# Kernel tuning notes

Measured on AMD Instinct MI355X. Metric: run time of the kernel, lower is better.

## Reference

```python
import jax, jax.numpy as jnp
import numpy as np

L, H, A, I, V, B, T = 6, 1024, 1024, 4096, 50277, 4, 2048
EPS = 1e-5
NEG = -1e38  # numerically equivalent to -inf init for the WKV exponent


def setup_inputs() -> dict:
    key = jax.random.key(0)
    ks = iter(jax.random.split(key, 32))
    def nrm(shape, s):
        return jax.random.normal(next(ks), shape, jnp.float32) * s
    def uni(shape):
        return jax.random.uniform(next(ks), shape, jnp.float32)
    inp = {
        'input_ids': jax.random.randint(next(ks), (B, T), 0, V),
        'embed': nrm((V, H), 0.02),
        'pre_ln_w': jnp.ones((H,), jnp.float32), 'pre_ln_b': jnp.zeros((H,), jnp.float32),
        'post_ln_w': jnp.ones((H,), jnp.float32), 'post_ln_b': jnp.zeros((H,), jnp.float32),
        'ln1_w': jnp.ones((L, H), jnp.float32), 'ln1_b': jnp.zeros((L, H), jnp.float32),
        'ln2_w': jnp.ones((L, H), jnp.float32), 'ln2_b': jnp.zeros((L, H), jnp.float32),
        'att_mix_k': uni((L, 1, 1, H)), 'att_mix_v': uni((L, 1, 1, H)), 'att_mix_r': uni((L, 1, 1, H)),
        'att_wk': nrm((L, A, H), H ** -0.5), 'att_wv': nrm((L, A, H), H ** -0.5),
        'att_wr': nrm((L, A, H), H ** -0.5), 'att_wo': nrm((L, H, A), A ** -0.5),
        'time_decay': nrm((L, A), 0.5), 'time_first': nrm((L, A), 0.5),
        'ffn_mix_k': uni((L, 1, 1, H)), 'ffn_mix_r': uni((L, 1, 1, H)),
        'ffn_wk': nrm((L, I, H), H ** -0.5), 'ffn_wr': nrm((L, H, H), H ** -0.5),
        'ffn_wv': nrm((L, H, I), I ** -0.5),
    }
    return inp


def layer_norm(x, w, b):
    mu = jnp.mean(x, axis=-1, keepdims=True)
    var = jnp.var(x, axis=-1, keepdims=True)
    return (x - mu) * jax.lax.rsqrt(var + EPS) * w + b


def time_shift(x):  # previous token, zero at t=0
    return jnp.pad(x, ((0, 0), (1, 0), (0, 0)))[:, :-1]


def wkv_scan(u, w, k, v):
    """RWKV WKV recurrence with max-exponent stabilization.
    u,w: [A]; k,v: [B,T,A] -> [B,T,A]."""
    def step(carry, kv):
        a, b, p = carry           # [B,A] each
        kt, vt = kv               # [B,A]
        q = jnp.maximum(p, u + kt)
        wt = jnp.exp(u + kt - q)
        sc = jnp.exp(p - q)
        out = (a * sc + wt * vt) / (b * sc + wt)
        q2 = jnp.maximum(p + w, kt)
        s1 = jnp.exp(p + w - q2)
        s2 = jnp.exp(kt - q2)
        return (s1 * a + s2 * vt, s1 * b + s2, q2), out
    bsz = k.shape[0]
    init = (jnp.zeros((bsz, A), k.dtype), jnp.zeros((bsz, A), k.dtype),
            jnp.full((bsz, A), NEG, k.dtype))
    _, out = jax.lax.scan(step, init, (k.transpose(1, 0, 2), v.transpose(1, 0, 2)))
    return out.transpose(1, 0, 2)


def reference(input_ids, embed, pre_ln_w, pre_ln_b, post_ln_w, post_ln_b,
              ln1_w, ln1_b, ln2_w, ln2_b,
              att_mix_k, att_mix_v, att_mix_r, att_wk, att_wv, att_wr, att_wo,
              time_decay, time_first, ffn_mix_k, ffn_mix_r, ffn_wk, ffn_wr, ffn_wv):
    h = layer_norm(embed[input_ids], pre_ln_w, pre_ln_b)
    for i in range(L):
        # --- attention (time mixing) ---
        x = layer_norm(h, ln1_w[i], ln1_b[i])
        prev = time_shift(x)
        k = (att_mix_k[i] * x + (1 - att_mix_k[i]) * prev) @ att_wk[i].T
        v = (att_mix_v[i] * x + (1 - att_mix_v[i]) * prev) @ att_wv[i].T
        r = jax.nn.sigmoid((att_mix_r[i] * x + (1 - att_mix_r[i]) * prev) @ att_wr[i].T)
        y = wkv_scan(time_first[i], -jnp.exp(time_decay[i]), k, v)
        h = h + (r * y) @ att_wo[i].T
        # --- feed forward (channel mixing) ---
        x = layer_norm(h, ln2_w[i], ln2_b[i])
        prev = time_shift(x)
        kk = jnp.square(jax.nn.relu((ffn_mix_k[i] * x + (1 - ffn_mix_k[i]) * prev) @ ffn_wk[i].T))
        rr = jax.nn.sigmoid((ffn_mix_r[i] * x + (1 - ffn_mix_r[i]) * prev) @ ffn_wr[i].T)
        h = h + rr * (kk @ ffn_wv[i].T)
    return layer_norm(h, post_ln_w, post_ln_b)
```

## Files before the change

### kernel.cpp

```cpp
#include <hip/hip_runtime.h>
#include <stdint.h>


#define LNUM 6
#define HD   1024
#define AD   1024
#define TT   2048
#define NTOK 8192
#define EPSF 1e-5f
#define NEGF (-1e38f)

#define WKV_C  32
#define WKV_NC 64
#define NCH    4096

typedef __attribute__((ext_vector_type(8))) short bf16x8;
typedef __attribute__((ext_vector_type(4))) float f32x4;

__device__ __forceinline__ unsigned short f2bf(float f) {
  union { float f; uint32_t u; } c; c.f = f;
  uint32_t r = c.u + 0x7fffu + ((c.u >> 16) & 1u);
  return (unsigned short)(r >> 16);
}

__device__ __forceinline__ void gld_lds16(const void* g, const void* l) {
  __builtin_amdgcn_global_load_lds(
      (const __attribute__((address_space(1))) void*)(uintptr_t)g,
      (__attribute__((address_space(3))) void*)(uint32_t)(uintptr_t)l,
      16, 0, 0);
}

enum { EP_NONE = 0, EP_SIG = 1, EP_RELUSQ = 2, EP_ADD = 3, EP_MULADD = 4, EP_KVR = 5 };

template <int EPI>
__global__ __launch_bounds__(256) void gemm_nt(
    const unsigned short* __restrict__ Aact,
    const unsigned short* __restrict__ Bw,
    float* __restrict__ Co,
    unsigned short* __restrict__ Cb,
    const float* __restrict__ aux,
    int K, int M)
{
  __shared__ unsigned short sA[4][128 * 32];
  __shared__ unsigned short sB[4][128 * 32];
  const int tid  = threadIdx.x;
  const int lane = tid & 63;
  const int wave = tid >> 6;
  const int quad = lane >> 4;
  const int r16  = lane & 15;
  const int wm = wave >> 1, wn = wave & 1;
  const int m0 = blockIdx.x * 128;
  const int n0 = blockIdx.y * 128;

  if constexpr (EPI == EP_KVR) {
    const int z = blockIdx.z;
    Aact += (size_t)z * 8388608;
    Bw   += (size_t)z * 1048576;
    Co   += (size_t)z * 8388608;
  }

  f32x4 acc[4][4];
#pragma unroll
  for (int i = 0; i < 4; ++i)
#pragma unroll
    for (int j = 0; j < 4; ++j) acc[i][j] = (f32x4){0.f, 0.f, 0.f, 0.f};

  const int wbase = wave * 64;
  const int nk = K >> 5;

  const int row0 = tid >> 2,         kc0 = tid & 3;
  const int row1 = 64 + row0,        kc1 = kc0;
  const int sw0 = (row0 >> 1) & 3;
  const int kg0 = kc0 ^ sw0;
  const int kg1 = kc1 ^ sw0;

  auto STAGE = [&](int buf, int kt) {
    const int k0 = kt << 5;
    gld_lds16(Aact + (size_t)(m0 + row0) * K + k0 + kg0 * 8,
              (const char*)sA[buf] + wbase * 16);
    gld_lds16(Bw   + (size_t)(n0 + row0) * K + k0 + kg0 * 8,
              (const char*)sB[buf] + wbase * 16);
    gld_lds16(Aact + (size_t)(m0 + row1) * K + k0 + kg1 * 8,
              (const char*)sA[buf] + (256 + wbase) * 16);
    gld_lds16(Bw   + (size_t)(n0 + row1) * K + k0 + kg1 * 8,
              (const char*)sB[buf] + (256 + wbase) * 16);
  };

  STAGE(0, 0);
  if (nk > 1) STAGE(1, 1);

  const int swr = (r16 >> 1) & 3;
  const int qsw = (quad ^ swr) * 8;

  for (int kt = 0; kt < nk; ++kt) {
    if (kt + 2 < nk) {
      STAGE((kt + 2) & 3, kt + 2);
      asm volatile("s_waitcnt vmcnt(8)" ::: "memory");
    } else if (kt + 1 < nk) {
      asm volatile("s_waitcnt vmcnt(4)" ::: "memory");
    } else {
      asm volatile("s_waitcnt vmcnt(0)" ::: "memory");
    }
    __builtin_amdgcn_s_barrier();
    asm volatile("" ::: "memory");

    const unsigned short* a_s = sA[kt & 3];
    const unsigned short* b_s = sB[kt & 3];
    bf16x8 af[4], bfr[4];
#pragma unroll
    for (int i = 0; i < 4; ++i) {
      af[i]  = *(const bf16x8*)(a_s + (wm * 64 + i * 16 + r16) * 32 + qsw);
      bfr[i] = *(const bf16x8*)(b_s + (wn * 64 + i * 16 + r16) * 32 + qsw);
    }
#pragma unroll
    for (int i = 0; i < 4; ++i)
#pragma unroll
      for (int j = 0; j < 4; ++j)
        acc[i][j] = __builtin_amdgcn_mfma_f32_16x16x32_bf16(af[i], bfr[j], acc[i][j], 0, 0, 0);
  }

#pragma unroll
  for (int i = 0; i < 4; ++i) {
    const int ar = m0 + wm * 64 + i * 16 + quad * 4;
#pragma unroll
    for (int j = 0; j < 4; ++j) {
      const int cc = n0 + wn * 64 + j * 16 + r16;
#pragma unroll
      for (int r = 0; r < 4; ++r) {
        const size_t idx = (size_t)(ar + r) * M + cc;
        const float v = acc[i][j][r];
        if constexpr (EPI == EP_NONE)   Co[idx] = v;
        if constexpr (EPI == EP_SIG)    Co[idx] = 1.f / (1.f + __expf(-v));
        if constexpr (EPI == EP_RELUSQ) { const float t = fmaxf(v, 0.f); Cb[idx] = f2bf(t * t); }
        if constexpr (EPI == EP_ADD)    Co[idx] += v;
        if constexpr (EPI == EP_MULADD) Co[idx] += aux[idx] * v;
        if constexpr (EPI == EP_KVR) {
          Co[idx] = (blockIdx.z == 2) ? (1.f / (1.f + __expf(-v))) : v;
        }
      }
    }
  }
}

__global__ __launch_bounds__(256) void ln_kernel(
    const float* __restrict__ in, const int* __restrict__ ids,
    const float* __restrict__ emb,
    const float* __restrict__ gw, const float* __restrict__ gb,
    float* __restrict__ out)
{
  const int n = blockIdx.x, tid = threadIdx.x;
  const float* src = ids ? (emb + (size_t)ids[n] * HD) : (in + (size_t)n * HD);
  const float4 v = ((const float4*)src)[tid];
  float s  = v.x + v.y + v.z + v.w;
  float s2 = v.x * v.x + v.y * v.y + v.z * v.z + v.w * v.w;
#pragma unroll
  for (int off = 32; off > 0; off >>= 1) {
    s  += __shfl_down(s, off);
    s2 += __shfl_down(s2, off);
  }
  __shared__ float red[8];
  const int wv = tid >> 6, ln = tid & 63;
  if (ln == 0) { red[wv] = s; red[4 + wv] = s2; }
  __syncthreads();
  if (tid == 0) {
    const float S  = red[0] + red[1] + red[2] + red[3];
    const float S2 = red[4] + red[5] + red[6] + red[7];
    const float mu = S * (1.f / HD);
    const float var = S2 * (1.f / HD) - mu * mu;
    red[0] = mu; red[1] = rsqrtf(var + EPSF);
  }
  __syncthreads();
  const float mu = red[0], rs = red[1];
  const float4 w4 = ((const float4*)gw)[tid];
  const float4 b4 = ((const float4*)gb)[tid];
  float4 o;
  o.x = (v.x - mu) * rs * w4.x + b4.x;
  o.y = (v.y - mu) * rs * w4.y + b4.y;
  o.z = (v.z - mu) * rs * w4.z + b4.z;
  o.w = (v.w - mu) * rs * w4.w + b4.w;
  ((float4*)(out + (size_t)n * HD))[tid] = o;
}

__global__ __launch_bounds__(256) void lnmix_kernel(
    const float* __restrict__ h,
    const float* __restrict__ gw, const float* __restrict__ gb,
    const float* __restrict__ m0p, const float* __restrict__ m1p, const float* __restrict__ m2p,
    ushort4* __restrict__ o0, ushort4* __restrict__ o1, ushort4* __restrict__ o2)
{
  const int n = blockIdx.x, tid = threadIdx.x;
  const int t = n & (TT - 1);
  const float4 vc = ((const float4*)(h + (size_t)n * HD))[tid];
  float4 vp = make_float4(0.f, 0.f, 0.f, 0.f);
  if (t != 0) vp = ((const float4*)(h + (size_t)(n - 1) * HD))[tid];

  float sc  = vc.x + vc.y + vc.z + vc.w;
  float sc2 = vc.x * vc.x + vc.y * vc.y + vc.z * vc.z + vc.w * vc.w;
  float sp  = vp.x + vp.y + vp.z + vp.w;
  float sp2 = vp.x * vp.x + vp.y * vp.y + vp.z * vp.z + vp.w * vp.w;
#pragma unroll
  for (int off = 32; off > 0; off >>= 1) {
    sc  += __shfl_down(sc, off);
    sc2 += __shfl_down(sc2, off);
    sp  += __shfl_down(sp, off);
    sp2 += __shfl_down(sp2, off);
  }
  __shared__ float red[16];
  const int wv = tid >> 6, ln = tid & 63;
  if (ln == 0) { red[wv] = sc; red[4 + wv] = sc2; red[8 + wv] = sp; red[12 + wv] = sp2; }
  __syncthreads();
  if (tid == 0) {
    float S  = red[0] + red[1] + red[2] + red[3];
    float S2 = red[4] + red[5] + red[6] + red[7];
    float mu = S * (1.f / HD);
    float var = S2 * (1.f / HD) - mu * mu;
    red[0] = mu; red[1] = rsqrtf(var + EPSF);
    S  = red[8] + red[9] + red[10] + red[11];
    S2 = red[12] + red[13] + red[14] + red[15];
    mu = S * (1.f / HD);
    var = S2 * (1.f / HD) - mu * mu;
    red[2] = mu; red[3] = rsqrtf(var + EPSF);
  }
  __syncthreads();
  const float muc = red[0], rsc = red[1];
  const float mup = red[2], rsp = red[3];
  const float4 w4 = ((const float4*)gw)[tid];
  const float4 b4 = ((const float4*)gb)[tid];
  float4 xc, xp;
  xc.x = (vc.x - muc) * rsc * w4.x + b4.x;
  xc.y = (vc.y - muc) * rsc * w4.y + b4.y;
  xc.z = (vc.z - muc) * rsc * w4.z + b4.z;
  xc.w = (vc.w - muc) * rsc * w4.w + b4.w;
  if (t != 0) {
    xp.x = (vp.x - mup) * rsp * w4.x + b4.x;
    xp.y = (vp.y - mup) * rsp * w4.y + b4.y;
    xp.z = (vp.z - mup) * rsp * w4.z + b4.z;
    xp.w = (vp.w - mup) * rsp * w4.w + b4.w;
  } else {
    xp = make_float4(0.f, 0.f, 0.f, 0.f);
  }

  const size_t o = (size_t)n * 256 + tid;
  float4 m = ((const float4*)m0p)[tid];
  ushort4 r;
  r.x = f2bf(m.x * xc.x + (1.f - m.x) * xp.x);
  r.y = f2bf(m.y * xc.y + (1.f - m.y) * xp.y);
  r.z = f2bf(m.z * xc.z + (1.f - m.z) * xp.z);
  r.w = f2bf(m.w * xc.w + (1.f - m.w) * xp.w);
  o0[o] = r;
  m = ((const float4*)m1p)[tid];
  r.x = f2bf(m.x * xc.x + (1.f - m.x) * xp.x);
  r.y = f2bf(m.y * xc.y + (1.f - m.y) * xp.y);
  r.z = f2bf(m.z * xc.z + (1.f - m.z) * xp.z);
  r.w = f2bf(m.w * xc.w + (1.f - m.w) * xp.w);
  o1[o] = r;
  if (o2) {
    m = ((const float4*)m2p)[tid];
    r.x = f2bf(m.x * xc.x + (1.f - m.x) * xp.x);
    r.y = f2bf(m.y * xc.y + (1.f - m.y) * xp.y);
    r.z = f2bf(m.z * xc.z + (1.f - m.z) * xp.z);
    r.w = f2bf(m.w * xc.w + (1.f - m.w) * xp.w);
    o2[o] = r;
  }
}

__global__ __launch_bounds__(256) void wkv_p1(
    const float* __restrict__ kx, const float* __restrict__ vx,
    const float* __restrict__ tdecay,
    float* __restrict__ la, float* __restrict__ lb, float* __restrict__ lp)
{
  const int c = blockIdx.x * 256 + threadIdx.x;
  const int a = c & (AD - 1);
  const int b = c >> 10;
  const int j = blockIdx.y;
  const float w = -__expf(tdecay[a]);
  const size_t base = ((size_t)b * TT + (size_t)j * WKV_C) * AD + a;
  float A = 0.f, Bb = 0.f, p = NEGF;
#pragma unroll 4
  for (int t = 0; t < WKV_C; ++t) {
    const float kt = kx[base + (size_t)t * AD];
    const float vt = vx[base + (size_t)t * AD];
    const float pn = fmaxf(p + w, kt);
    const float s1 = __expf(p + w - pn);
    const float s2 = __expf(kt - pn);
    A = s1 * A + s2 * vt;
    Bb = s1 * Bb + s2;
    p = pn;
  }
  const int o = j * NCH + c;
  la[o] = A; lb[o] = Bb; lp[o] = p;
}

__global__ __launch_bounds__(256) void wkv_p2(
    const float* __restrict__ la, const float* __restrict__ lb,
    const float* __restrict__ lp, const float* __restrict__ tdecay,
    float* __restrict__ sa, float* __restrict__ sb, float* __restrict__ sp)
{
  const int c = blockIdx.x * 256 + threadIdx.x;
  const int a = c & (AD - 1);
  const float wC = -__expf(tdecay[a]) * (float)WKV_C;
  float A = 0.f, Bb = 0.f, p = NEGF;
  for (int j = 0; j < WKV_NC; ++j) {
    const int o = j * NCH + c;
    sa[o] = A; sb[o] = Bb; sp[o] = p;
    const float A2 = la[o], B2 = lb[o], p2 = lp[o];
    const float pn = fmaxf(p + wC, p2);
    const float e1 = __expf(p + wC - pn);
    const float e2 = __expf(p2 - pn);
    A = e1 * A + e2 * A2;
    Bb = e1 * Bb + e2 * B2;
    p = pn;
  }
}

__global__ __launch_bounds__(256) void wkv_p3(
    const float* __restrict__ kx, const float* __restrict__ vx,
    const float* __restrict__ rx,
    const float* __restrict__ tfirst, const float* __restrict__ tdecay,
    const float* __restrict__ sa, const float* __restrict__ sb,
    const float* __restrict__ sp,
    unsigned short* __restrict__ ry)
{
  const int c = blockIdx.x * 256 + threadIdx.x;
  const int a = c & (AD - 1);
  const int b = c >> 10;
  const int j = blockIdx.y;
  const float u = tfirst[a];
  const float w = -__expf(tdecay[a]);
  const size_t base = ((size_t)b * TT + (size_t)j * WKV_C) * AD + a;
  const int o = j * NCH + c;
  float A = sa[o], Bb = sb[o], p = sp[o];
#pragma unroll 2
  for (int t = 0; t < WKV_C; ++t) {
    const size_t off = base + (size_t)t * AD;
    const float kt = kx[off], vt = vx[off];
    const float q  = fmaxf(p, u + kt);
    const float wt = __expf(u + kt - q);
    const float sc = __expf(p - q);
    const float y  = (A * sc + wt * vt) / (Bb * sc + wt);
    ry[off] = f2bf(y * rx[off]);
    const float pn = fmaxf(p + w, kt);
    const float s1 = __expf(p + w - pn);
    const float s2 = __expf(kt - pn);
    A = s1 * A + s2 * vt;
    Bb = s1 * Bb + s2;
    p = pn;
  }
}

__global__ __launch_bounds__(256) void f2b7_kernel(
    const float* __restrict__ s0, const float* __restrict__ s1,
    const float* __restrict__ s2, const float* __restrict__ s3,
    const float* __restrict__ s4, const float* __restrict__ s5,
    const float* __restrict__ s6, ushort4* __restrict__ wb4)
{
  const size_t i = (size_t)blockIdx.x * 256 + threadIdx.x;
  const float* s; size_t rel;
  if      (i <  262144) { s = s0; rel = i; }
  else if (i <  524288) { s = s1; rel = i -  262144; }
  else if (i <  786432) { s = s2; rel = i -  524288; }
  else if (i < 1048576) { s = s3; rel = i -  786432; }
  else if (i < 2097152) { s = s4; rel = i - 1048576; }
  else if (i < 2359296) { s = s5; rel = i - 2097152; }
  else                  { s = s6; rel = i - 2359296; }
  const float4 v = ((const float4*)s)[rel];
  ushort4 r;
  r.x = f2bf(v.x); r.y = f2bf(v.y); r.z = f2bf(v.z); r.w = f2bf(v.w);
  wb4[i] = r;
}

extern "C" void kernel_launch(void* const* d_in, const int* in_sizes, int n_in,
                              void* d_out, int out_size, void* d_ws, size_t ws_size,
                              hipStream_t stream)
{
  (void)in_sizes; (void)n_in; (void)out_size; (void)ws_size;
  const int*   ids   = (const int*)d_in[0];
  const float* emb   = (const float*)d_in[1];
  const float* prew  = (const float*)d_in[2];
  const float* preb  = (const float*)d_in[3];
  const float* postw = (const float*)d_in[4];
  const float* postb = (const float*)d_in[5];
  const float* ln1w  = (const float*)d_in[6];
  const float* ln1b  = (const float*)d_in[7];
  const float* ln2w  = (const float*)d_in[8];
  const float* ln2b  = (const float*)d_in[9];
  const float* amk   = (const float*)d_in[10];
  const float* amv   = (const float*)d_in[11];
  const float* amr   = (const float*)d_in[12];
  const float* awk   = (const float*)d_in[13];
  const float* awv   = (const float*)d_in[14];
  const float* awr   = (const float*)d_in[15];
  const float* awo   = (const float*)d_in[16];
  const float* td    = (const float*)d_in[17];
  const float* tf    = (const float*)d_in[18];
  const float* fmk   = (const float*)d_in[19];
  const float* fmr   = (const float*)d_in[20];
  const float* fwk   = (const float*)d_in[21];
  const float* fwr   = (const float*)d_in[22];
  const float* fwv   = (const float*)d_in[23];

  char* ws = (char*)d_ws;
  float* h  = (float*)(ws + 0);
  float* x  = (float*)(ws + 33554432);
  float* kb = (float*)(ws + 67108864);
  float* vb = (float*)(ws + 100663296);
  float* rb = (float*)(ws + 134217728);
  unsigned short* ab = (unsigned short*)(ws + 167772160);
  unsigned short* wb = (unsigned short*)(ws + 234881024);

  unsigned short* xk = ab;
  unsigned short* xv = ab + 8388608;
  unsigned short* xr = ab + 16777216;
  unsigned short* ry = ab + 25165824;

  float* wla = x;
  float* wlb = x + WKV_NC * NCH;
  float* wlp = x + 2 * WKV_NC * NCH;
  float* wsa = x + 3 * WKV_NC * NCH;
  float* wsb = x + 4 * WKV_NC * NCH;
  float* wsp = x + 5 * WKV_NC * NCH;

  const dim3 blk(256);
  const dim3 g1(NTOK / 128, 1024 / 128);
  const dim3 g2(NTOK / 128, 4096 / 128);
  const dim3 gkvr(NTOK / 128, 1024 / 128, 3);
  const dim3 gw(NCH / 256, WKV_NC);

  ln_kernel<<<NTOK, blk, 0, stream>>>(nullptr, ids, emb, prew, preb, h);

  for (int i = 0; i < LNUM; ++i) {
    f2b7_kernel<<<13312, blk, 0, stream>>>(
        awk + (size_t)i * 1048576, awv + (size_t)i * 1048576,
        awr + (size_t)i * 1048576, awo + (size_t)i * 1048576,
        fwk + (size_t)i * 4194304, fwr + (size_t)i * 1048576,
        fwv + (size_t)i * 4194304, (ushort4*)wb);

    lnmix_kernel<<<NTOK, blk, 0, stream>>>(h, ln1w + i * HD, ln1b + i * HD,
                                           amk + i * HD, amv + i * HD, amr + i * HD,
                                           (ushort4*)xk, (ushort4*)xv, (ushort4*)xr);
    gemm_nt<EP_KVR><<<gkvr, blk, 0, stream>>>(xk, wb, kb, nullptr, nullptr, 1024, 1024);
    wkv_p1<<<gw, blk, 0, stream>>>(kb, vb, td + i * AD, wla, wlb, wlp);
    wkv_p2<<<NCH / 256, blk, 0, stream>>>(wla, wlb, wlp, td + i * AD, wsa, wsb, wsp);
    wkv_p3<<<gw, blk, 0, stream>>>(kb, vb, rb, tf + i * AD, td + i * AD, wsa, wsb, wsp, ry);
    gemm_nt<EP_ADD ><<<g1, blk, 0, stream>>>(ry, wb + 3145728, h, nullptr, nullptr, 1024, 1024);

    lnmix_kernel<<<NTOK, blk, 0, stream>>>(h, ln2w + i * HD, ln2b + i * HD,
                                           fmk + i * HD, fmr + i * HD, nullptr,
                                           (ushort4*)kb, (ushort4*)vb, nullptr);
    gemm_nt<EP_RELUSQ><<<g2, blk, 0, stream>>>((unsigned short*)kb, wb + 4194304, nullptr, ab, nullptr, 1024, 4096);
    gemm_nt<EP_SIG   ><<<g1, blk, 0, stream>>>((unsigned short*)vb, wb + 8388608, rb, nullptr, nullptr, 1024, 1024);
    gemm_nt<EP_MULADD><<<g1, blk, 0, stream>>>(ab, wb + 9437184, h, nullptr, rb, 4096, 1024);
  }

  ln_kernel<<<NTOK, blk, 0, stream>>>(h, nullptr, nullptr, postw, postb, (float*)d_out);
}
```

Baseline: 2.750 ms.

## Use 512-thread GEMM blocks and merge FFN key and receptance GEMMs

The GEMM kernel moves from 256 to 512 threads per 128x128 tile, so each wave computes a 64x32 sub-tile and each thread issues one staging load per operand per k-step, with the vmcnt waits adjusted to match. The aim is more waves per tile to hide latency and fewer accumulator registers per thread. Separately, the FFN relu-squared key GEMM and the sigmoid receptance GEMM are merged into a single launch, with blockIdx.y selecting the operand offsets and epilogue, which saves a launch and lets both fill the device together. The cost is lower MFMA-per-LDS-read reuse per wave and a branchy epilogue.

```diff
diff --git a/kernel.cpp b/kernel.cpp
--- a/kernel.cpp
+++ b/kernel.cpp
@@ -30,10 +30,11 @@
       16, 0, 0);
 }
 
-enum { EP_NONE = 0, EP_SIG = 1, EP_RELUSQ = 2, EP_ADD = 3, EP_MULADD = 4, EP_KVR = 5 };
+enum { EP_NONE = 0, EP_SIG = 1, EP_RELUSQ = 2, EP_ADD = 3, EP_MULADD = 4,
+       EP_KVR = 5, EP_FKR = 6 };
 
 template <int EPI>
-__global__ __launch_bounds__(256) void gemm_nt(
+__global__ __launch_bounds__(512, 4) void gemm_nt(
     const unsigned short* __restrict__ Aact,
     const unsigned short* __restrict__ Bw,
     float* __restrict__ Co,
@@ -48,56 +49,60 @@
   const int wave = tid >> 6;
   const int quad = lane >> 4;
   const int r16  = lane & 15;
-  const int wm = wave >> 1, wn = wave & 1;
+  const int wm = wave >> 2, wn = wave & 3;
   const int m0 = blockIdx.x * 128;
-  const int n0 = blockIdx.y * 128;
-
+  int n0 = blockIdx.y * 128;
+
+  bool sig = false;
   if constexpr (EPI == EP_KVR) {
     const int z = blockIdx.z;
     Aact += (size_t)z * 8388608;
     Bw   += (size_t)z * 1048576;
     Co   += (size_t)z * 8388608;
   }
-
-  f32x4 acc[4][4];
+  if constexpr (EPI == EP_FKR) {
+    if (blockIdx.y >= 32) {
+      sig = true;
+      Aact += 16777216;
+      Bw   += 4194304;
+      n0   = (blockIdx.y - 32) * 128;
+      M    = 1024;
+    } else {
+      M = 4096;
+    }
+  }
+
+  f32x4 acc[4][2];
 #pragma unroll
   for (int i = 0; i < 4; ++i)
 #pragma unroll
-    for (int j = 0; j < 4; ++j) acc[i][j] = (f32x4){0.f, 0.f, 0.f, 0.f};
-
-  const int wbase = wave * 64;
+    for (int j = 0; j < 2; ++j) acc[i][j] = (f32x4){0.f, 0.f, 0.f, 0.f};
+
   const int nk = K >> 5;
 
-  const int row0 = tid >> 2,         kc0 = tid & 3;
-  const int row1 = 64 + row0,        kc1 = kc0;
-  const int sw0 = (row0 >> 1) & 3;
-  const int kg0 = kc0 ^ sw0;
-  const int kg1 = kc1 ^ sw0;
+  const int row0 = tid >> 2, kc0 = tid & 3;
+  const int kg0  = kc0 ^ ((row0 >> 1) & 3);
+  const int wbase = wave * 64 * 16;
 
   auto STAGE = [&](int buf, int kt) {
     const int k0 = kt << 5;
     gld_lds16(Aact + (size_t)(m0 + row0) * K + k0 + kg0 * 8,
-              (const char*)sA[buf] + wbase * 16);
+              (const char*)sA[buf] + wbase);
     gld_lds16(Bw   + (size_t)(n0 + row0) * K + k0 + kg0 * 8,
-              (const char*)sB[buf] + wbase * 16);
-    gld_lds16(Aact + (size_t)(m0 + row1) * K + k0 + kg1 * 8,
-              (const char*)sA[buf] + (256 + wbase) * 16);
-    gld_lds16(Bw   + (size_t)(n0 + row1) * K + k0 + kg1 * 8,
-              (const char*)sB[buf] + (256 + wbase) * 16);
+              (const char*)sB[buf] + wbase);
   };
 
   STAGE(0, 0);
   if (nk > 1) STAGE(1, 1);
 
-  const int swr = (r16 >> 1) & 3;
-  const int qsw = (quad ^ swr) * 8;
+  const int qsw = (quad ^ ((r16 >> 1) & 3)) * 8;
 
   for (int kt = 0; kt < nk; ++kt) {
     if (kt + 2 < nk) {
       STAGE((kt + 2) & 3, kt + 2);
-      asm volatile("s_waitcnt vmcnt(8)" ::: "memory");
+      asm volatile("s_waitcnt vmcnt(4)" ::: "memory");
     } else if (kt + 1 < nk) {
-      asm volatile("s_waitcnt vmcnt(4)" ::: "memory");
+      asm volatile("s_waitcnt vmcnt(2)" ::: "memory");
     } else {
       asm volatile("s_waitcnt vmcnt(0)" ::: "memory");
     }
@@ -106,16 +111,17 @@
 
     const unsigned short* a_s = sA[kt & 3];
     const unsigned short* b_s = sB[kt & 3];
-    bf16x8 af[4], bfr[4];
-#pragma unroll
-    for (int i = 0; i < 4; ++i) {
+    bf16x8 af[4], bfr[2];
+#pragma unroll
+    for (int i = 0; i < 4; ++i)
       af[i]  = *(const bf16x8*)(a_s + (wm * 64 + i * 16 + r16) * 32 + qsw);
-      bfr[i] = *(const bf16x8*)(b_s + (wn * 64 + i * 16 + r16) * 32 + qsw);
-    }
+#pragma unroll
+    for (int j = 0; j < 2; ++j)
+      bfr[j] = *(const bf16x8*)(b_s + (wn * 32 + j * 16 + r16) * 32 + qsw);
 #pragma unroll
     for (int i = 0; i < 4; ++i)
 #pragma unroll
-      for (int j = 0; j < 4; ++j)
+      for (int j = 0; j < 2; ++j)
         acc[i][j] = __builtin_amdgcn_mfma_f32_16x16x32_bf16(af[i], bfr[j], acc[i][j], 0, 0, 0);
   }
 
@@ -123,8 +129,8 @@
   for (int i = 0; i < 4; ++i) {
     const int ar = m0 + wm * 64 + i * 16 + quad * 4;
 #pragma unroll
-    for (int j = 0; j < 4; ++j) {
-      const int cc = n0 + wn * 64 + j * 16 + r16;
+    for (int j = 0; j < 2; ++j) {
+      const int cc = n0 + wn * 32 + j * 16 + r16;
 #pragma unroll
       for (int r = 0; r < 4; ++r) {
         const size_t idx = (size_t)(ar + r) * M + cc;
@@ -134,8 +140,11 @@
         if constexpr (EPI == EP_RELUSQ) { const float t = fmaxf(v, 0.f); Cb[idx] = f2bf(t * t); }
         if constexpr (EPI == EP_ADD)    Co[idx] += v;
         if constexpr (EPI == EP_MULADD) Co[idx] += aux[idx] * v;
-        if constexpr (EPI == EP_KVR) {
+        if constexpr (EPI == EP_KVR)
           Co[idx] = (blockIdx.z == 2) ? (1.f / (1.f + __expf(-v))) : v;
+        if constexpr (EPI == EP_FKR) {
+          if (sig) Co[idx] = 1.f / (1.f + __expf(-v));
+          else     { const float t = fmaxf(v, 0.f); Cb[idx] = f2bf(t * t); }
         }
       }
     }
@@ -420,9 +429,10 @@
   float* wsp = x + 5 * WKV_NC * NCH;
 
   const dim3 blk(256);
+  const dim3 gblk(512);
   const dim3 g1(NTOK / 128, 1024 / 128);
-  const dim3 g2(NTOK / 128, 4096 / 128);
   const dim3 gkvr(NTOK / 128, 1024 / 128, 3);
+  const dim3 gffn(NTOK / 128, 40);
   const dim3 gw(NCH / 256, WKV_NC);
 
   ln_kernel<<<NTOK, blk, 0, stream>>>(nullptr, ids, emb, prew, preb, h);
@@ -437,18 +447,17 @@
     lnmix_kernel<<<NTOK, blk, 0, stream>>>(h, ln1w + i * HD, ln1b + i * HD,
                                            amk + i * HD, amv + i * HD, amr + i * HD,
                                            (ushort4*)xk, (ushort4*)xv, (ushort4*)xr);
-    gemm_nt<EP_KVR><<<gkvr, blk, 0, stream>>>(xk, wb, kb, nullptr, nullptr, 1024, 1024);
+    gemm_nt<EP_KVR><<<gkvr, gblk, 0, stream>>>(xk, wb, kb, nullptr, nullptr, 1024, 1024);
     wkv_p1<<<gw, blk, 0, stream>>>(kb, vb, td + i * AD, wla, wlb, wlp);
     wkv_p2<<<NCH / 256, blk, 0, stream>>>(wla, wlb, wlp, td + i * AD, wsa, wsb, wsp);
     wkv_p3<<<gw, blk, 0, stream>>>(kb, vb, rb, tf + i * AD, td + i * AD, wsa, wsb, wsp, ry);
-    gemm_nt<EP_ADD ><<<g1, blk, 0, stream>>>(ry, wb + 3145728, h, nullptr, nullptr, 1024, 1024);
+    gemm_nt<EP_ADD ><<<g1, gblk, 0, stream>>>(ry, wb + 3145728, h, nullptr, nullptr, 1024, 1024);
 
     lnmix_kernel<<<NTOK, blk, 0, stream>>>(h, ln2w + i * HD, ln2b + i * HD,
                                            fmk + i * HD, fmr + i * HD, nullptr,
                                            (ushort4*)kb, (ushort4*)vb, nullptr);
-    gemm_nt<EP_RELUSQ><<<g2, blk, 0, stream>>>((unsigned short*)kb, wb + 4194304, nullptr, ab, nullptr, 1024, 4096);
-    gemm_nt<EP_SIG   ><<<g1, blk, 0, stream>>>((unsigned short*)vb, wb + 8388608, rb, nullptr, nullptr, 1024, 1024);
-    gemm_nt<EP_MULADD><<<g1, blk, 0, stream>>>(ab, wb + 9437184, h, nullptr, rb, 4096, 1024);
+    gemm_nt<EP_FKR   ><<<gffn, gblk, 0, stream>>>((unsigned short*)kb, wb + 4194304, rb, ab, nullptr, 1024, 0);
+    gemm_nt<EP_MULADD><<<g1,   gblk, 0, stream>>>(ab, wb + 9437184, h, nullptr, rb, 4096, 1024);
   }
 
   ln_kernel<<<NTOK, blk, 0, stream>>>(h, nullptr, nullptr, postw, postb, (float*)d_out);
```

New measurement: 2.693 ms. 1.02x faster.
